# Optimization experiments

Hardware: AMD Instinct MI355X
Metric: run time of the kernel (lower is better)

Reference implementation:

```python
import jax, jax.numpy as jnp
import numpy as np

N, E, D, H = 100000, 1600000, 128, 2  # nodes, edges, channels (in=out), heads
NEG_SLOPE = 0.2
EPS = 1e-16


def setup_inputs() -> dict:
    key = jax.random.key(0)
    ks = jax.random.split(key, 12)
    s = 1.0 / np.sqrt(D)
    return {
        "x": jax.random.normal(ks[0], (N, D), jnp.float32),
        "edge_index": jax.random.randint(ks[1], (2, E), 0, N, jnp.int64),
        "gamma": jnp.ones((D,), jnp.float32),
        "beta": jnp.zeros((D,), jnp.float32),
        "Wl": jax.random.normal(ks[2], (D, H * D), jnp.float32) * s,
        "bl": jnp.zeros((H * D,), jnp.float32),
        "Wr": jax.random.normal(ks[3], (D, H * D), jnp.float32) * s,
        "br": jnp.zeros((H * D,), jnp.float32),
        "att": jax.random.normal(ks[4], (H, D), jnp.float32) * s,
        "res_W": jax.random.normal(ks[5], (D, D), jnp.float32) * s,
        "bias": jnp.zeros((D,), jnp.float32),
    }


def _segment_softmax(alpha, seg, num_segments):
    m = jax.ops.segment_max(alpha, seg, num_segments=num_segments)
    a = jnp.exp(alpha - m[seg])
    z = jax.ops.segment_sum(a, seg, num_segments=num_segments)
    return a / (z[seg] + EPS)


def reference(x, edge_index, gamma, beta, Wl, bl, Wr, br, att, res_W, bias):
    n = x.shape[0]
    residual = x
    # per-node LayerNorm -> ReLU
    mu = x.mean(-1, keepdims=True)
    var = ((x - mu) ** 2).mean(-1, keepdims=True)
    h = (x - mu) * jax.lax.rsqrt(var + 1e-5) * gamma + beta
    h = jax.nn.relu(h)
    # GATv2: per-node linear transforms [N,H,D]
    xl = (h @ Wl + bl).reshape(n, H, D)  # source-side
    xr = (h @ Wr + br).reshape(n, H, D)  # target-side
    src, dst = edge_index[0], edge_index[1]
    e = jax.nn.leaky_relu(xl[src] + xr[dst], NEG_SLOPE)  # [E,H,D]
    alpha = jnp.einsum('ehd,hd->eh', e, att)             # [E,H]
    alpha = _segment_softmax(alpha, dst, n)
    msg = xl[src] * alpha[..., None]                     # [E,H,D]
    out = jax.ops.segment_sum(msg, dst, num_segments=n)  # [N,H,D]
    out = out.mean(axis=1)                               # concat=False -> mean heads
    out = out + h @ res_W + bias                         # GATv2 internal residual + bias
    return residual + out
```

## Files before the change

kernel.cpp:

```cpp
#include <hip/hip_runtime.h>
#include <hip/hip_bf16.h>
#include <cstdint>
#include <cstddef>

#define DCH 128
#define NHEADS 2
#define NEG_SLOPE 0.2f

typedef __attribute__((ext_vector_type(8))) short short8v;
typedef __attribute__((ext_vector_type(4))) float f32x4;
typedef __attribute__((ext_vector_type(2))) float f32x2;
typedef _Float16 h4 __attribute__((ext_vector_type(4)));

__device__ __forceinline__ unsigned short f2bf(float f) {
    union { float f; unsigned int i; } v; v.f = f;
    unsigned int r = v.i + 0x7fffu + ((v.i >> 16) & 1u);
    return (unsigned short)(r >> 16);
}
__device__ __forceinline__ unsigned short f2h_bits(float f) {
    _Float16 h = (_Float16)f;
    union { _Float16 h; unsigned short u; } v; v.h = h; return v.u;
}

__device__ __forceinline__ float halfsum(float p) {
    p += __int_as_float(__builtin_amdgcn_update_dpp(
            0, __float_as_int(p), 0x121, 0xF, 0xF, false));
    p += __int_as_float(__builtin_amdgcn_update_dpp(
            0, __float_as_int(p), 0x122, 0xF, 0xF, false));
    p += __int_as_float(__builtin_amdgcn_update_dpp(
            0, __float_as_int(p), 0x124, 0xF, 0xF, false));
    p += __int_as_float(__builtin_amdgcn_update_dpp(
            0, __float_as_int(p), 0x128, 0xF, 0xF, false));
    p += __int_as_float(__builtin_amdgcn_ds_swizzle(
            __float_as_int(p), 0x401F));
    return p;
}

__global__ void prep_and_zero(const float* __restrict__ Wl, const float* __restrict__ Wr,
                              const float* __restrict__ resW,
                              unsigned short* __restrict__ wfrag,
                              int* __restrict__ cnt, int n) {
    if (blockIdx.x >= 40) {
        int i = (blockIdx.x - 40) * 256 + threadIdx.x;
        if (i < n) cnt[i] = 0;
        return;
    }
    int gid  = blockIdx.x * 256 + threadIdx.x;
    int lane = gid & 63;
    int f    = gid >> 6;
    int ks   = f & 3;
    int ct   = f >> 2;
    int col  = ct * 16 + (lane & 15);
    int k0   = ks * 32 + (lane >> 4) * 8;
    const float* W; int ldB, c;
    if (col < 256)      { W = Wl;   ldB = 256; c = col; }
    else if (col < 512) { W = Wr;   ldB = 256; c = col - 256; }
    else                { W = resW; ldB = 128; c = col - 512; }
    unsigned short tmp[8];
#pragma unroll
    for (int j = 0; j < 8; ++j) tmp[j] = f2bf(W[(size_t)(k0 + j) * ldB + c]);
    ushort4* dst = (ushort4*)(wfrag + (size_t)gid * 8);
    dst[0] = make_ushort4(tmp[0], tmp[1], tmp[2], tmp[3]);
    dst[1] = make_ushort4(tmp[4], tmp[5], tmp[6], tmp[7]);
}

__launch_bounds__(256)
__global__ void gemm_fill(const float* __restrict__ x,
                          const float* __restrict__ gamma, const float* __restrict__ beta,
                          const unsigned short* __restrict__ wfrag,
                          const float* __restrict__ bl, const float* __restrict__ br,
                          const float* __restrict__ bias,
                          unsigned char* __restrict__ xl8, unsigned short* __restrict__ xr,
                          float* __restrict__ out, int n,
                          const int* __restrict__ srcIdx, const int* __restrict__ dstIdx,
                          int* __restrict__ fillc, int* __restrict__ sbuf, int E, int nrb) {
    __shared__ __align__(16) unsigned char smem[128 * 256];

    if ((int)blockIdx.x >= 3 * nrb) {
        int i = (blockIdx.x - 3 * nrb) * 256 + threadIdx.x;
        int E4 = E >> 2;
        if (i < E4) {
            int4 d = ((const int4*)dstIdx)[i];
            int4 s = ((const int4*)srcIdx)[i];
            sbuf[atomicAdd(&fillc[d.x], 1)] = s.x;
            sbuf[atomicAdd(&fillc[d.y], 1)] = s.y;
            sbuf[atomicAdd(&fillc[d.z], 1)] = s.z;
            sbuf[atomicAdd(&fillc[d.w], 1)] = s.w;
        }
        if (i < (E & 3)) {
            int e = E4 * 4 + i;
            sbuf[atomicAdd(&fillc[dstIdx[e]], 1)] = srcIdx[e];
        }
        return;
    }

    int sec  = blockIdx.x / nrb;
    int rb   = blockIdx.x % nrb;
    int row0 = rb * 128;
    int tid  = threadIdx.x;
    unsigned short* As = (unsigned short*)smem;

    {
        int r  = tid >> 5;
        int k4 = (tid & 31) * 4;
        float4 g4  = *(const float4*)(gamma + k4);
        float4 be4 = *(const float4*)(beta + k4);
#pragma unroll
        for (int i = 0; i < 16; ++i) {
            int row  = r + i * 8;
            int grow = row0 + row;
            float4 a = (grow < n) ? *(const float4*)(x + (size_t)grow * DCH + k4)
                                  : make_float4(0.f, 0.f, 0.f, 0.f);
            float s  = a.x + a.y + a.z + a.w;
            float sq = a.x * a.x + a.y * a.y + a.z * a.z + a.w * a.w;
#pragma unroll
            for (int msk = 16; msk; msk >>= 1) {
                s  += __shfl_xor(s, msk);
                sq += __shfl_xor(sq, msk);
            }
            float mu = s * (1.f / DCH);
            float rs = rsqrtf(sq * (1.f / DCH) - mu * mu + 1e-5f);
            ushort4 u;
            u.x = f2bf(fmaxf((a.x - mu) * rs * g4.x + be4.x, 0.f));
            u.y = f2bf(fmaxf((a.y - mu) * rs * g4.y + be4.y, 0.f));
            u.z = f2bf(fmaxf((a.z - mu) * rs * g4.z + be4.z, 0.f));
            u.w = f2bf(fmaxf((a.w - mu) * rs * g4.w + be4.w, 0.f));
            int byteoff = row * 256 + ((k4 * 2) ^ ((row & 7) << 4));
            *(ushort4*)((char*)As + byteoff) = u;
        }
    }
    __syncthreads();

    int wv = tid >> 6, lane = tid & 63;

    short8v afrag[2][4];
#pragma unroll
    for (int g = 0; g < 2; ++g) {
        int arow = wv * 32 + g * 16 + (lane & 15);
#pragma unroll
        for (int ks = 0; ks < 4; ++ks) {
            int kbyte = (ks * 64 + (lane >> 4) * 16) ^ ((arow & 7) << 4);
            afrag[g][ks] = *(const short8v*)((const char*)As + arow * 256 + kbyte);
        }
    }
    __syncthreads();

    int nodeL0 = wv * 32 + (lane & 15);
    int nodeL1 = nodeL0 + 16;
    int cq = (lane >> 4) << 2;

    auto mfma_ct = [&](int ct, f32x4& a0, f32x4& a1) {
        const unsigned short* bp = wfrag + ((size_t)(ct * 4) * 64 + lane) * 8;
        short8v b0 = *(const short8v*)(bp);
        short8v b1 = *(const short8v*)(bp + 64 * 8);
        short8v b2 = *(const short8v*)(bp + 128 * 8);
        short8v b3 = *(const short8v*)(bp + 192 * 8);
        a0 = __builtin_amdgcn_mfma_f32_16x16x32_bf16(b0, afrag[0][0], a0, 0, 0, 0);
        a1 = __builtin_amdgcn_mfma_f32_16x16x32_bf16(b0, afrag[1][0], a1, 0, 0, 0);
        a0 = __builtin_amdgcn_mfma_f32_16x16x32_bf16(b1, afrag[0][1], a0, 0, 0, 0);
        a1 = __builtin_amdgcn_mfma_f32_16x16x32_bf16(b1, afrag[1][1], a1, 0, 0, 0);
        a0 = __builtin_amdgcn_mfma_f32_16x16x32_bf16(b2, afrag[0][2], a0, 0, 0, 0);
        a1 = __builtin_amdgcn_mfma_f32_16x16x32_bf16(b2, afrag[1][2], a1, 0, 0, 0);
        a0 = __builtin_amdgcn_mfma_f32_16x16x32_bf16(b3, afrag[0][3], a0, 0, 0, 0);
        a1 = __builtin_amdgcn_mfma_f32_16x16x32_bf16(b3, afrag[1][3], a1, 0, 0, 0);
    };

    if (sec == 0) {
#pragma unroll
        for (int ct = 0; ct < 16; ++ct) {
            f32x4 a0 = {0,0,0,0}, a1 = {0,0,0,0};
            mfma_ct(ct, a0, a1);
            int c = ct * 16 + cq;
            float4 bb = *(const float4*)(bl + c);
            int cb = ct * 16 + cq;
            int p0 = __builtin_amdgcn_cvt_pk_fp8_f32(a0[0] + bb.x, a0[1] + bb.y, 0, false);
            p0     = __builtin_amdgcn_cvt_pk_fp8_f32(a0[2] + bb.z, a0[3] + bb.w, p0, true);
            *(int*)(smem + nodeL0 * 256 + (cb ^ ((nodeL0 & 7) << 4))) = p0;
            int p1 = __builtin_amdgcn_cvt_pk_fp8_f32(a1[0] + bb.x, a1[1] + bb.y, 0, false);
            p1     = __builtin_amdgcn_cvt_pk_fp8_f32(a1[2] + bb.z, a1[3] + bb.w, p1, true);
            *(int*)(smem + nodeL1 * 256 + (cb ^ ((nodeL1 & 7) << 4))) = p1;
        }
        __syncthreads();
#pragma unroll
        for (int it = 0; it < 8; ++it) {
            int chunk = it * 256 + tid;
            int row  = chunk >> 4;
            int colb = (chunk & 15) * 16;
            int grow = row0 + row;
            if (grow < n) {
                int4 v = *(const int4*)(smem + row * 256 + (colb ^ ((row & 7) << 4)));
                *(int4*)(xl8 + (size_t)grow * 256 + colb) = v;
            }
        }
    } else if (sec == 1) {
        for (int fg = 0; fg < 2; ++fg) {
#pragma unroll
            for (int ctl = 0; ctl < 8; ++ctl) {
                int ct = 16 + fg * 8 + ctl;
                f32x4 a0 = {0,0,0,0}, a1 = {0,0,0,0};
                mfma_ct(ct, a0, a1);
                int c = ct * 16 + cq - 256;
                float4 bb = *(const float4*)(br + c);
                int cb = ctl * 32 + cq * 2;
                ushort4 u0 = make_ushort4(f2h_bits(a0[0] + bb.x), f2h_bits(a0[1] + bb.y),
                                          f2h_bits(a0[2] + bb.z), f2h_bits(a0[3] + bb.w));
                *(ushort4*)(smem + nodeL0 * 256 + (cb ^ ((nodeL0 & 7) << 4))) = u0;
                ushort4 u1 = make_ushort4(f2h_bits(a1[0] + bb.x), f2h_bits(a1[1] + bb.y),
                                          f2h_bits(a1[2] + bb.z), f2h_bits(a1[3] + bb.w));
                *(ushort4*)(smem + nodeL1 * 256 + (cb ^ ((nodeL1 & 7) << 4))) = u1;
            }
            __syncthreads();
#pragma unroll
            for (int it = 0; it < 8; ++it) {
                int chunk = it * 256 + tid;
                int row  = chunk >> 4;
                int colb = (chunk & 15) * 16;
                int grow = row0 + row;
                if (grow < n) {
                    int4 v = *(const int4*)(smem + row * 256 + (colb ^ ((row & 7) << 4)));
                    *(int4*)((char*)xr + (size_t)grow * 512 + fg * 256 + colb) = v;
                }
            }
            __syncthreads();
        }
    } else {
        for (int fg = 0; fg < 2; ++fg) {
#pragma unroll
            for (int ctl = 0; ctl < 4; ++ctl) {
                int ct = 32 + fg * 4 + ctl;
                f32x4 a0 = {0,0,0,0}, a1 = {0,0,0,0};
                mfma_ct(ct, a0, a1);
                int c = ct * 16 + cq - 512;
                float4 bb = *(const float4*)(bias + c);
                int cb = ctl * 64 + cq * 4;
                float4 w0 = make_float4(a0[0] + bb.x, a0[1] + bb.y,
                                        a0[2] + bb.z, a0[3] + bb.w);
                *(float4*)(smem + nodeL0 * 256 + (cb ^ ((nodeL0 & 7) << 4))) = w0;
                float4 w1 = make_float4(a1[0] + bb.x, a1[1] + bb.y,
                                        a1[2] + bb.z, a1[3] + bb.w);
                *(float4*)(smem + nodeL1 * 256 + (cb ^ ((nodeL1 & 7) << 4))) = w1;
            }
            __syncthreads();
#pragma unroll
            for (int it = 0; it < 8; ++it) {
                int chunk = it * 256 + tid;
                int row  = chunk >> 4;
                int colb = (chunk & 15) * 16;
                int grow = row0 + row;
                if (grow < n) {
                    float4 v = *(const float4*)(smem + row * 256 + (colb ^ ((row & 7) << 4)));
                    float4 xv = *(const float4*)((const char*)x + (size_t)grow * 512 + fg * 256 + colb);
                    v.x += xv.x; v.y += xv.y; v.z += xv.z; v.w += xv.w;
                    *(float4*)((char*)out + (size_t)grow * 512 + fg * 256 + colb) = v;
                }
            }
            __syncthreads();
        }
    }
}

__global__ void hist_dst(const int* __restrict__ dst, int* __restrict__ cnt, int E) {
    int i = blockIdx.x * blockDim.x + threadIdx.x;
    int E4 = E >> 2;
    if (i < E4) {
        int4 d = ((const int4*)dst)[i];
        atomicAdd(&cnt[d.x], 1); atomicAdd(&cnt[d.y], 1);
        atomicAdd(&cnt[d.z], 1); atomicAdd(&cnt[d.w], 1);
    }
    if (i < (E & 3)) atomicAdd(&cnt[dst[E4 * 4 + i]], 1);
}

__global__ void scan_block(const int* __restrict__ cnt, int* __restrict__ offs,
                           int* __restrict__ bsum, int n) {
    __shared__ int sm[256];
    int t = threadIdx.x;
    int i = blockIdx.x * 256 + t;
    int v = (i < n) ? cnt[i] : 0;
    sm[t] = v;
    __syncthreads();
#pragma unroll
    for (int d = 1; d < 256; d <<= 1) {
        int add = (t >= d) ? sm[t - d] : 0;
        __syncthreads();
        sm[t] += add;
        __syncthreads();
    }
    if (i < n) offs[i] = sm[t] - v;
    if (t == 255) bsum[blockIdx.x] = sm[t];
}

__global__ void scan_bsum_par(int* __restrict__ bsum, int nb) {
    __shared__ int sm[512];
    int t = threadIdx.x;
    if (nb <= 512) {
        int v = (t < nb) ? bsum[t] : 0;
        sm[t] = v;
        __syncthreads();
#pragma unroll
        for (int d = 1; d < 512; d <<= 1) {
            int add = (t >= d) ? sm[t - d] : 0;
            __syncthreads();
            sm[t] += add;
            __syncthreads();
        }
        if (t < nb) bsum[t] = sm[t] - v;
    } else if (t == 0) {
        int acc = 0;
        for (int i = 0; i < nb; ++i) { int v = bsum[i]; bsum[i] = acc; acc += v; }
    }
}

__global__ void scan_add(int* __restrict__ offs, int* __restrict__ fillc,
                         const int* __restrict__ bsum, int n, int E) {
    int i = blockIdx.x * 256 + threadIdx.x;
    if (i < n) {
        int v = offs[i] + bsum[blockIdx.x];
        offs[i]  = v;
        fillc[i] = v;
    }
    if (i == 0) offs[n] = E;
}

__launch_bounds__(256)
__global__ void gat_aggregate(const int* __restrict__ offs, const int* __restrict__ sbuf,
                              const unsigned char* __restrict__ xl8,
                              const unsigned short* __restrict__ xr_,
                              const float* __restrict__ att,
                              float* __restrict__ out, int n) {
    const _Float16* xr = (const _Float16*)xr_;
    int lane = threadIdx.x & 63;
    int wid  = __builtin_amdgcn_readfirstlane((blockIdx.x * blockDim.x + threadIdx.x) >> 6);
    int nw   = (gridDim.x * blockDim.x) >> 6;

    const float LOG2E = 1.4426950408889634f;
    float4 af = *(const float4*)(att + lane * 4);
    float ax = af.x * LOG2E, ay = af.y * LOG2E, az = af.z * LOG2E, aw = af.w * LOG2E;

    for (int t = wid; t < n; t += nw) {
        int beg = offs[t];
        int end = offs[t + 1];
        if (beg == end) continue;
        h4 rr = *(const h4*)(xr + (size_t)t * 256 + lane * 4);
        float rx = (float)rr[0], ry = (float)rr[1], rz = (float)rr[2], rw = (float)rr[3];

        float m = -INFINITY, z = 0.f;
        float4 acc = make_float4(0.f, 0.f, 0.f, 0.f);

        auto process4 = [&](int u0, int u1, int u2, int u3) {
            f32x2 l0a = __builtin_amdgcn_cvt_pk_f32_fp8(u0, false);
            f32x2 l0b = __builtin_amdgcn_cvt_pk_f32_fp8(u0, true);
            f32x2 l1a = __builtin_amdgcn_cvt_pk_f32_fp8(u1, false);
            f32x2 l1b = __builtin_amdgcn_cvt_pk_f32_fp8(u1, true);
            f32x2 l2a = __builtin_amdgcn_cvt_pk_f32_fp8(u2, false);
            f32x2 l2b = __builtin_amdgcn_cvt_pk_f32_fp8(u2, true);
            f32x2 l3a = __builtin_amdgcn_cvt_pk_f32_fp8(u3, false);
            f32x2 l3b = __builtin_amdgcn_cvt_pk_f32_fp8(u3, true);

            auto logit = [&](f32x2 la, f32x2 lb) {
                float vx = la.x + rx; vx = fmaxf(vx, NEG_SLOPE * vx);
                float vy = la.y + ry; vy = fmaxf(vy, NEG_SLOPE * vy);
                float vz = lb.x + rz; vz = fmaxf(vz, NEG_SLOPE * vz);
                float vw = lb.y + rw; vw = fmaxf(vw, NEG_SLOPE * vw);
                return fmaf(vw, aw, fmaf(vz, az, fmaf(vy, ay, vx * ax)));
            };
            float p0 = halfsum(logit(l0a, l0b));
            float p1 = halfsum(logit(l1a, l1b));
            float p2 = halfsum(logit(l2a, l2b));
            float p3 = halfsum(logit(l3a, l3b));
            float pm = fmaxf(fmaxf(p0, p1), fmaxf(p2, p3));
            if (__any(pm - m > 11.5f)) {
                float mn = fmaxf(m, pm);
                float sc = __builtin_amdgcn_exp2f(m - mn);
                z *= sc;
                acc.x *= sc; acc.y *= sc; acc.z *= sc; acc.w *= sc;
                m = mn;
            }
            float w0 = __builtin_amdgcn_exp2f(p0 - m);
            float w1 = __builtin_amdgcn_exp2f(p1 - m);
            float w2 = __builtin_amdgcn_exp2f(p2 - m);
            float w3 = __builtin_amdgcn_exp2f(p3 - m);
            z += (w0 + w1) + (w2 + w3);
            acc.x = fmaf(l0a.x, w0, acc.x); acc.y = fmaf(l0a.y, w0, acc.y);
            acc.z = fmaf(l0b.x, w0, acc.z); acc.w = fmaf(l0b.y, w0, acc.w);
            acc.x = fmaf(l1a.x, w1, acc.x); acc.y = fmaf(l1a.y, w1, acc.y);
            acc.z = fmaf(l1b.x, w1, acc.z); acc.w = fmaf(l1b.y, w1, acc.w);
            acc.x = fmaf(l2a.x, w2, acc.x); acc.y = fmaf(l2a.y, w2, acc.y);
            acc.z = fmaf(l2b.x, w2, acc.z); acc.w = fmaf(l2b.y, w2, acc.w);
            acc.x = fmaf(l3a.x, w3, acc.x); acc.y = fmaf(l3a.y, w3, acc.y);
            acc.z = fmaf(l3b.x, w3, acc.z); acc.w = fmaf(l3b.y, w3, acc.w);
        };

        int j = beg;
        int c0, c1, c2, c3;
        bool have = (j + 4 <= end);
        if (have) {
            int s0 = sbuf[j], s1 = sbuf[j + 1], s2 = sbuf[j + 2], s3 = sbuf[j + 3];
            c0 = *(const int*)(xl8 + (size_t)s0 * 256 + lane * 4);
            c1 = *(const int*)(xl8 + (size_t)s1 * 256 + lane * 4);
            c2 = *(const int*)(xl8 + (size_t)s2 * 256 + lane * 4);
            c3 = *(const int*)(xl8 + (size_t)s3 * 256 + lane * 4);
        }
        for (; j + 8 <= end; j += 4) {
            int s0 = sbuf[j + 4], s1 = sbuf[j + 5], s2 = sbuf[j + 6], s3 = sbuf[j + 7];
            int n0 = *(const int*)(xl8 + (size_t)s0 * 256 + lane * 4);
            int n1 = *(const int*)(xl8 + (size_t)s1 * 256 + lane * 4);
            int n2 = *(const int*)(xl8 + (size_t)s2 * 256 + lane * 4);
            int n3 = *(const int*)(xl8 + (size_t)s3 * 256 + lane * 4);
            process4(c0, c1, c2, c3);
            c0 = n0; c1 = n1; c2 = n2; c3 = n3;
        }
        if (have) { process4(c0, c1, c2, c3); j += 4; }
        for (; j < end; ++j) {
            int u = *(const int*)(xl8 + (size_t)sbuf[j] * 256 + lane * 4);
            f32x2 la = __builtin_amdgcn_cvt_pk_f32_fp8(u, false);
            f32x2 lb = __builtin_amdgcn_cvt_pk_f32_fp8(u, true);
            float vx = la.x + rx; vx = fmaxf(vx, NEG_SLOPE * vx);
            float vy = la.y + ry; vy = fmaxf(vy, NEG_SLOPE * vy);
            float vz = lb.x + rz; vz = fmaxf(vz, NEG_SLOPE * vz);
            float vw = lb.y + rw; vw = fmaxf(vw, NEG_SLOPE * vw);
            float p = halfsum(fmaf(vw, aw, fmaf(vz, az, fmaf(vy, ay, vx * ax))));
            if (__any(p - m > 11.5f)) {
                float mn = fmaxf(m, p);
                float sc = __builtin_amdgcn_exp2f(m - mn);
                z *= sc;
                acc.x *= sc; acc.y *= sc; acc.z *= sc; acc.w *= sc;
                m = mn;
            }
            float w = __builtin_amdgcn_exp2f(p - m);
            z += w;
            acc.x = fmaf(la.x, w, acc.x); acc.y = fmaf(la.y, w, acc.y);
            acc.z = fmaf(lb.x, w, acc.z); acc.w = fmaf(lb.y, w, acc.w);
        }
        float inv = 0.5f / (z + 1e-16f);
        acc.x *= inv; acc.y *= inv; acc.z *= inv; acc.w *= inv;
        acc.x += __shfl_xor(acc.x, 32);
        acc.y += __shfl_xor(acc.y, 32);
        acc.z += __shfl_xor(acc.z, 32);
        acc.w += __shfl_xor(acc.w, 32);
        if (lane < 32) {
            float4* o = (float4*)(out + (size_t)t * DCH + lane * 4);
            float4 cur = *o;
            cur.x += acc.x; cur.y += acc.y; cur.z += acc.z; cur.w += acc.w;
            *o = cur;
        }
    }
}

extern "C" void kernel_launch(void* const* d_in, const int* in_sizes, int n_in,
                              void* d_out, int out_size, void* d_ws, size_t ws_size,
                              hipStream_t stream) {
    const float* x     = (const float*)d_in[0];
    const int*   ei    = (const int*)d_in[1];
    const float* gamma = (const float*)d_in[2];
    const float* beta  = (const float*)d_in[3];
    const float* Wl    = (const float*)d_in[4];
    const float* bl    = (const float*)d_in[5];
    const float* Wr    = (const float*)d_in[6];
    const float* br    = (const float*)d_in[7];
    const float* att   = (const float*)d_in[8];
    const float* resW  = (const float*)d_in[9];
    const float* bias  = (const float*)d_in[10];
    float* out = (float*)d_out;

    int n = in_sizes[0] / DCH;
    int E = in_sizes[1] / 2;
    const int* src = ei;
    const int* dstIdx = ei + E;

    char* ws = (char*)d_ws;
    size_t off = 0;
    auto alloc = [&](size_t bytes) -> void* {
        void* p = ws + off;
        off = (off + bytes + 255) & ~(size_t)255;
        return p;
    };

    int nb = (n + 255) / 256;

    unsigned char*  xl8 = (unsigned char*)alloc((size_t)n * 256);
    unsigned short* xr  = (unsigned short*)alloc((size_t)n * 256 * 2);
    unsigned short* wfrag = (unsigned short*)alloc(160 * 64 * 8 * 2);
    int* cnt   = (int*)alloc((size_t)n * 4);
    int* offs  = (int*)alloc((size_t)(n + 1) * 4);
    int* bsum  = (int*)alloc((size_t)nb * 4);
    int* fillc = (int*)alloc((size_t)n * 4);
    int* sbuf  = (int*)alloc((size_t)E * 4);

    prep_and_zero<<<40 + nb, 256, 0, stream>>>(Wl, Wr, resW, wfrag, cnt, n);
    int ethr = (E / 4 + 255) / 256 + 1;
    hist_dst<<<ethr, 256, 0, stream>>>(dstIdx, cnt, E);
    scan_block<<<nb, 256, 0, stream>>>(cnt, offs, bsum, n);
    scan_bsum_par<<<1, 512, 0, stream>>>(bsum, nb);
    scan_add<<<nb, 256, 0, stream>>>(offs, fillc, bsum, n, E);

    int nrb = (n + 127) / 128;
    gemm_fill<<<3 * nrb + ethr, 256, 0, stream>>>(x, gamma, beta, wfrag, bl, br, bias,
                                                  xl8, xr, out, n,
                                                  src, dstIdx, fillc, sbuf, E, nrb);
    gat_aggregate<<<2048, 256, 0, stream>>>(offs, sbuf, xl8, xr, att, out, n);
}
```

Measured before the change: 340.1 us.

## Merge GEMM sections into one block per row tile; fuse histogram with weight prep

Each gemm_fill block now computes the xl, xr and residual outputs for its 128-row tile in sequence, instead of launching three blocks per tile that each redo the LayerNorm and A-fragment load. The destination histogram is folded into the weight-prep kernel, and the count buffer is cleared with a memset. xr and out are written with nontemporal stores. This removes redundant LayerNorm work and one kernel launch, at the cost of fewer but longer GEMM blocks and less parallelism across sections.

```diff
diff --git a/kernel.cpp b/kernel.cpp
--- a/kernel.cpp
+++ b/kernel.cpp
@@ -10,6 +10,7 @@
 typedef __attribute__((ext_vector_type(8))) short short8v;
 typedef __attribute__((ext_vector_type(4))) float f32x4;
 typedef __attribute__((ext_vector_type(2))) float f32x2;
+typedef __attribute__((ext_vector_type(4))) int int4v;
 typedef _Float16 h4 __attribute__((ext_vector_type(4)));
 
 __device__ __forceinline__ unsigned short f2bf(float f) {
@@ -36,13 +37,19 @@
     return p;
 }
 
-__global__ void prep_and_zero(const float* __restrict__ Wl, const float* __restrict__ Wr,
-                              const float* __restrict__ resW,
-                              unsigned short* __restrict__ wfrag,
-                              int* __restrict__ cnt, int n) {
+__global__ void prep_hist(const float* __restrict__ Wl, const float* __restrict__ Wr,
+                          const float* __restrict__ resW,
+                          unsigned short* __restrict__ wfrag,
+                          const int* __restrict__ dst, int* __restrict__ cnt, int E) {
     if (blockIdx.x >= 40) {
         int i = (blockIdx.x - 40) * 256 + threadIdx.x;
-        if (i < n) cnt[i] = 0;
+        int E4 = E >> 2;
+        if (i < E4) {
+            int4 d = ((const int4*)dst)[i];
+            atomicAdd(&cnt[d.x], 1); atomicAdd(&cnt[d.y], 1);
+            atomicAdd(&cnt[d.z], 1); atomicAdd(&cnt[d.w], 1);
+        }
+        if (i < (E & 3)) atomicAdd(&cnt[dst[E4 * 4 + i]], 1);
         return;
     }
     int gid  = blockIdx.x * 256 + threadIdx.x;
@@ -59,9 +66,9 @@
     unsigned short tmp[8];
 #pragma unroll
     for (int j = 0; j < 8; ++j) tmp[j] = f2bf(W[(size_t)(k0 + j) * ldB + c]);
-    ushort4* dst = (ushort4*)(wfrag + (size_t)gid * 8);
-    dst[0] = make_ushort4(tmp[0], tmp[1], tmp[2], tmp[3]);
-    dst[1] = make_ushort4(tmp[4], tmp[5], tmp[6], tmp[7]);
+    ushort4* dstp = (ushort4*)(wfrag + (size_t)gid * 8);
+    dstp[0] = make_ushort4(tmp[0], tmp[1], tmp[2], tmp[3]);
+    dstp[1] = make_ushort4(tmp[4], tmp[5], tmp[6], tmp[7]);
 }
 
 __launch_bounds__(256)
@@ -76,8 +83,8 @@
                           int* __restrict__ fillc, int* __restrict__ sbuf, int E, int nrb) {
     __shared__ __align__(16) unsigned char smem[128 * 256];
 
-    if ((int)blockIdx.x >= 3 * nrb) {
-        int i = (blockIdx.x - 3 * nrb) * 256 + threadIdx.x;
+    if ((int)blockIdx.x >= nrb) {
+        int i = (blockIdx.x - nrb) * 256 + threadIdx.x;
         int E4 = E >> 2;
         if (i < E4) {
             int4 d = ((const int4*)dstIdx)[i];
@@ -94,9 +101,7 @@
         return;
     }
 
-    int sec  = blockIdx.x / nrb;
-    int rb   = blockIdx.x % nrb;
-    int row0 = rb * 128;
+    int row0 = blockIdx.x * 128;
     int tid  = threadIdx.x;
     unsigned short* As = (unsigned short*)smem;
 
@@ -165,7 +170,7 @@
         a1 = __builtin_amdgcn_mfma_f32_16x16x32_bf16(b3, afrag[1][3], a1, 0, 0, 0);
     };
 
-    if (sec == 0) {
+    {
 #pragma unroll
         for (int ct = 0; ct < 16; ++ct) {
             f32x4 a0 = {0,0,0,0}, a1 = {0,0,0,0};
@@ -188,86 +193,79 @@
             int colb = (chunk & 15) * 16;
             int grow = row0 + row;
             if (grow < n) {
-                int4 v = *(const int4*)(smem + row * 256 + (colb ^ ((row & 7) << 4)));
-                *(int4*)(xl8 + (size_t)grow * 256 + colb) = v;
-            }
-        }
-    } else if (sec == 1) {
-        for (int fg = 0; fg < 2; ++fg) {
-#pragma unroll
-            for (int ctl = 0; ctl < 8; ++ctl) {
-                int ct = 16 + fg * 8 + ctl;
-                f32x4 a0 = {0,0,0,0}, a1 = {0,0,0,0};
-                mfma_ct(ct, a0, a1);
-                int c = ct * 16 + cq - 256;
-                float4 bb = *(const float4*)(br + c);
-                int cb = ctl * 32 + cq * 2;
-                ushort4 u0 = make_ushort4(f2h_bits(a0[0] + bb.x), f2h_bits(a0[1] + bb.y),
-                                          f2h_bits(a0[2] + bb.z), f2h_bits(a0[3] + bb.w));
-                *(ushort4*)(smem + nodeL0 * 256 + (cb ^ ((nodeL0 & 7) << 4))) = u0;
-                ushort4 u1 = make_ushort4(f2h_bits(a1[0] + bb.x), f2h_bits(a1[1] + bb.y),
-                                          f2h_bits(a1[2] + bb.z), f2h_bits(a1[3] + bb.w));
-                *(ushort4*)(smem + nodeL1 * 256 + (cb ^ ((nodeL1 & 7) << 4))) = u1;
-            }
-            __syncthreads();
-#pragma unroll
-            for (int it = 0; it < 8; ++it) {
-                int chunk = it * 256 + tid;
-                int row  = chunk >> 4;
-                int colb = (chunk & 15) * 16;
-                int grow = row0 + row;
-                if (grow < n) {
-                    int4 v = *(const int4*)(smem + row * 256 + (colb ^ ((row & 7) << 4)));
-                    *(int4*)((char*)xr + (size_t)grow * 512 + fg * 256 + colb) = v;
-                }
-            }
-            __syncthreads();
-        }
-    } else {
-        for (int fg = 0; fg < 2; ++fg) {
-#pragma unroll
-            for (int ctl = 0; ctl < 4; ++ctl) {
-                int ct = 32 + fg * 4 + ctl;
-                f32x4 a0 = {0,0,0,0}, a1 = {0,0,0,0};
-                mfma_ct(ct, a0, a1);
-                int c = ct * 16 + cq - 512;
-                float4 bb = *(const float4*)(bias + c);
-                int cb = ctl * 64 + cq * 4;
-                float4 w0 = make_float4(a0[0] + bb.x, a0[1] + bb.y,
-                                        a0[2] + bb.z, a0[3] + bb.w);
-                *(float4*)(smem + nodeL0 * 256 + (cb ^ ((nodeL0 & 7) << 4))) = w0;
-                float4 w1 = make_float4(a1[0] + bb.x, a1[1] + bb.y,
-                                        a1[2] + bb.z, a1[3] + bb.w);
-                *(float4*)(smem + nodeL1 * 256 + (cb ^ ((nodeL1 & 7) << 4))) = w1;
-            }
-            __syncthreads();
-#pragma unroll
-            for (int it = 0; it < 8; ++it) {
-                int chunk = it * 256 + tid;
-                int row  = chunk >> 4;
-                int colb = (chunk & 15) * 16;
-                int grow = row0 + row;
-                if (grow < n) {
-                    float4 v = *(const float4*)(smem + row * 256 + (colb ^ ((row & 7) << 4)));
-                    float4 xv = *(const float4*)((const char*)x + (size_t)grow * 512 + fg * 256 + colb);
-                    v.x += xv.x; v.y += xv.y; v.z += xv.z; v.w += xv.w;
-                    *(float4*)((char*)out + (size_t)grow * 512 + fg * 256 + colb) = v;
-                }
-            }
-            __syncthreads();
-        }
-    }
-}
-
-__global__ void hist_dst(const int* __restrict__ dst, int* __restrict__ cnt, int E) {
-    int i = blockIdx.x * blockDim.x + threadIdx.x;
-    int E4 = E >> 2;
-    if (i < E4) {
-        int4 d = ((const int4*)dst)[i];
-        atomicAdd(&cnt[d.x], 1); atomicAdd(&cnt[d.y], 1);
-        atomicAdd(&cnt[d.z], 1); atomicAdd(&cnt[d.w], 1);
-    }
-    if (i < (E & 3)) atomicAdd(&cnt[dst[E4 * 4 + i]], 1);
+                int4v v = *(const int4v*)(smem + row * 256 + (colb ^ ((row & 7) << 4)));
+                *(int4v*)(xl8 + (size_t)grow * 256 + colb) = v;
+            }
+        }
+        __syncthreads();
+    }
+
+    for (int fg = 0; fg < 2; ++fg) {
+#pragma unroll
+        for (int ctl = 0; ctl < 8; ++ctl) {
+            int ct = 16 + fg * 8 + ctl;
+            f32x4 a0 = {0,0,0,0}, a1 = {0,0,0,0};
+            mfma_ct(ct, a0, a1);
+            int c = ct * 16 + cq - 256;
+            float4 bb = *(const float4*)(br + c);
+            int cb = ctl * 32 + cq * 2;
+            ushort4 u0 = make_ushort4(f2h_bits(a0[0] + bb.x), f2h_bits(a0[1] + bb.y),
+                                      f2h_bits(a0[2] + bb.z), f2h_bits(a0[3] + bb.w));
+            *(ushort4*)(smem + nodeL0 * 256 + (cb ^ ((nodeL0 & 7) << 4))) = u0;
+            ushort4 u1 = make_ushort4(f2h_bits(a1[0] + bb.x), f2h_bits(a1[1] + bb.y),
+                                      f2h_bits(a1[2] + bb.z), f2h_bits(a1[3] + bb.w));
+            *(ushort4*)(smem + nodeL1 * 256 + (cb ^ ((nodeL1 & 7) << 4))) = u1;
+        }
+        __syncthreads();
+#pragma unroll
+        for (int it = 0; it < 8; ++it) {
+            int chunk = it * 256 + tid;
+            int row  = chunk >> 4;
+            int colb = (chunk & 15) * 16;
+            int grow = row0 + row;
+            if (grow < n) {
+                int4v v = *(const int4v*)(smem + row * 256 + (colb ^ ((row & 7) << 4)));
+                __builtin_nontemporal_store(v,
+                    (int4v*)((char*)xr + (size_t)grow * 512 + fg * 256 + colb));
+            }
+        }
+        __syncthreads();
+    }
+
+    for (int fg = 0; fg < 2; ++fg) {
+#pragma unroll
+        for (int ctl = 0; ctl < 4; ++ctl) {
+            int ct = 32 + fg * 4 + ctl;
+            f32x4 a0 = {0,0,0,0}, a1 = {0,0,0,0};
+            mfma_ct(ct, a0, a1);
+            int c = ct * 16 + cq - 512;
+            float4 bb = *(const float4*)(bias + c);
+            int cb = ctl * 64 + cq * 4;
+            float4 w0 = make_float4(a0[0] + bb.x, a0[1] + bb.y,
+                                    a0[2] + bb.z, a0[3] + bb.w);
+            *(float4*)(smem + nodeL0 * 256 + (cb ^ ((nodeL0 & 7) << 4))) = w0;
+            float4 w1 = make_float4(a1[0] + bb.x, a1[1] + bb.y,
+                                    a1[2] + bb.z, a1[3] + bb.w);
+            *(float4*)(smem + nodeL1 * 256 + (cb ^ ((nodeL1 & 7) << 4))) = w1;
+        }
+        __syncthreads();
+#pragma unroll
+        for (int it = 0; it < 8; ++it) {
+            int chunk = it * 256 + tid;
+            int row  = chunk >> 4;
+            int colb = (chunk & 15) * 16;
+            int grow = row0 + row;
+            if (grow < n) {
+                f32x4 v = *(const f32x4*)(smem + row * 256 + (colb ^ ((row & 7) << 4)));
+                const float* xp = (const float*)((const char*)x + (size_t)grow * 512 + fg * 256 + colb);
+                f32x4 xv = *(const f32x4*)xp;
+                v = v + xv;
+                __builtin_nontemporal_store(v,
+                    (f32x4*)((char*)out + (size_t)grow * 512 + fg * 256 + colb));
+            }
+        }
+        __syncthreads();
+    }
 }
 
 __global__ void scan_block(const int* __restrict__ cnt, int* __restrict__ offs,
@@ -486,16 +484,16 @@
     int* fillc = (int*)alloc((size_t)n * 4);
     int* sbuf  = (int*)alloc((size_t)E * 4);
 
-    prep_and_zero<<<40 + nb, 256, 0, stream>>>(Wl, Wr, resW, wfrag, cnt, n);
+    (void)hipMemsetAsync(cnt, 0, (size_t)n * 4, stream);
     int ethr = (E / 4 + 255) / 256 + 1;
-    hist_dst<<<ethr, 256, 0, stream>>>(dstIdx, cnt, E);
+    prep_hist<<<40 + ethr, 256, 0, stream>>>(Wl, Wr, resW, wfrag, dstIdx, cnt, E);
     scan_block<<<nb, 256, 0, stream>>>(cnt, offs, bsum, n);
     scan_bsum_par<<<1, 512, 0, stream>>>(bsum, nb);
     scan_add<<<nb, 256, 0, stream>>>(offs, fillc, bsum, n, E);
 
     int nrb = (n + 127) / 128;
-    gemm_fill<<<3 * nrb + ethr, 256, 0, stream>>>(x, gamma, beta, wfrag, bl, br, bias,
-                                                  xl8, xr, out, n,
-                                                  src, dstIdx, fillc, sbuf, E, nrb);
+    gemm_fill<<<nrb + ethr, 256, 0, stream>>>(x, gamma, beta, wfrag, bl, br, bias,
+                                              xl8, xr, out, n,
+                                              src, dstIdx, fillc, sbuf, E, nrb);
     gat_aggregate<<<2048, 256, 0, stream>>>(offs, sbuf, xl8, xr, att, out, n);
 }
```

After: 294.0 us. -13.5%, faster.
